# Kernel tuning notes

Hardware: AMD Instinct MI355X
Metric: run time of the kernel (lower is better)

Reference implementation:

```python
import jax, jax.numpy as jnp
import numpy as np
import math

B, S, D, H = 4, 2048, 512, 8
DK = D // H
EPS = 1e-6

def _xavier(key, shape):
    fan_in, fan_out = shape[1], shape[0]
    a = math.sqrt(6.0 / (fan_in + fan_out))
    return jax.random.uniform(key, shape, jnp.float32, -a, a)

def setup_inputs() -> dict:
    key = jax.random.key(0)
    ks = jax.random.split(key, 8)
    return {
        "x_q": jax.random.normal(ks[0], (B, S, D), jnp.float32),
        "x_k": jax.random.normal(ks[1], (B, S, D), jnp.float32),
        "Wq": _xavier(ks[2], (D, D)),
        "Wk": _xavier(ks[3], (D, D)),
        "Wv": _xavier(ks[4], (D, D)),
        "Wg": jnp.zeros((D, D), jnp.float32),      # gating weight init to 0
        "bg": jnp.ones((D,), jnp.float32),          # gating bias init to 1
        "Wo": _xavier(ks[5], (D, D)),
        "bo": jnp.zeros((D,), jnp.float32),
        "gamma": jnp.ones((D,), jnp.float32),
        "beta": jnp.zeros((D,), jnp.float32),
    }

def _ln(x, gamma, beta):
    mu = jnp.mean(x, axis=-1, keepdims=True)
    var = jnp.var(x, axis=-1, keepdims=True)
    return (x - mu) * jax.lax.rsqrt(var + EPS) * gamma + beta

def reference(x_q, x_k, Wq, Wk, Wv, Wg, bg, Wo, bo, gamma, beta):
    xq = _ln(x_q, gamma, beta)          # [B,S,D]
    xk = _ln(x_k, gamma, beta)
    q = xq @ Wq.T                        # nn.Linear: x @ W^T (no bias)
    k = xk @ Wk.T
    v = xk @ Wv.T
    q = q.reshape(B, S, H, DK)
    k = k.reshape(B, S, H, DK)
    v = v.reshape(B, S, H, DK)
    attn = jnp.einsum('bshd,bthd->bhst', q, k) / math.sqrt(DK)  # [B,H,S,S]
    attn = jax.nn.softmax(attn, axis=-1) * jax.nn.softmax(attn, axis=-2)
    out = jnp.einsum('bhst,bthd->bshd', attn, v).reshape(B, S, D)
    gate = jax.nn.sigmoid(xq @ Wg.T + bg)
    return (out * gate) @ Wo.T + bo
```

## Files before the change

kernel.cpp:

```cpp
#include <hip/hip_runtime.h>

#define BB 4
#define SS 2048
#define DD 512
#define HH 8
#define RR (BB * SS)
#define BH (BB * HH)

typedef unsigned short u16;
typedef unsigned int   u32;
typedef __attribute__((ext_vector_type(4))) float f32x4;
typedef __attribute__((ext_vector_type(8))) short bf16x8;

__device__ __forceinline__ float bf2f(u16 u) { return __uint_as_float(((u32)u) << 16); }
__device__ __forceinline__ u16 f2bf(float f) {
    u32 x = __float_as_uint(f);
    return (u16)((x + 0x7fffu + ((x >> 16) & 1u)) >> 16);
}
__device__ __forceinline__ bool is_bf16(const void* gamma) {
    return *(const u32*)gamma == 0x3F803F80u;
}
__device__ __forceinline__ float ldin(const void* p, size_t i, bool b16) {
    return b16 ? bf2f(((const u16*)p)[i]) : ((const float*)p)[i];
}
__device__ __forceinline__ float expc(float x) { return __expf(fminf(x, 60.f)); }

__global__ __launch_bounds__(256) void k_ln(
    const void* xq, const void* xk, const void* gamma, const void* beta,
    u16* __restrict__ lnq, u16* __restrict__ lnk, float* l_col)
{
    bool b16 = is_bf16(gamma);
    int row = blockIdx.x, tid = threadIdx.x;
    const void* x = blockIdx.y ? xk : xq;
    u16* o = blockIdx.y ? lnk : lnq;
    size_t base = (size_t)row * DD;

    if (blockIdx.y == 0 && row < 256) l_col[row * 256 + tid] = 0.f;

    float x0 = ldin(x, base + tid * 2, b16);
    float x1 = ldin(x, base + tid * 2 + 1, b16);
    float s = x0 + x1, ss = x0 * x0 + x1 * x1;
    for (int m = 1; m < 64; m <<= 1) { s += __shfl_xor(s, m); ss += __shfl_xor(ss, m); }
    __shared__ float ws4[4], wss4[4], mu_s, rs_s;
    int wv = tid >> 6;
    if ((tid & 63) == 0) { ws4[wv] = s; wss4[wv] = ss; }
    __syncthreads();
    if (tid == 0) {
        float S1 = ws4[0] + ws4[1] + ws4[2] + ws4[3];
        float S2 = wss4[0] + wss4[1] + wss4[2] + wss4[3];
        float mu = S1 / (float)DD;
        float var = S2 / (float)DD - mu * mu;
        mu_s = mu; rs_s = rsqrtf(fmaxf(var, 0.f) + 1e-6f);
    }
    __syncthreads();
    float mu = mu_s, rstd = rs_s;
    float g0 = ldin(gamma, tid * 2, b16), g1 = ldin(gamma, tid * 2 + 1, b16);
    float b0 = ldin(beta, tid * 2, b16),  b1 = ldin(beta, tid * 2 + 1, b16);
    o[base + tid * 2]     = f2bf((x0 - mu) * rstd * g0 + b0);
    o[base + tid * 2 + 1] = f2bf((x1 - mu) * rstd * g1 + b1);
}

__global__ __launch_bounds__(256) void k_proj4(
    const u16* __restrict__ lnq, const u16* __restrict__ lnk,
    const void* Wq, const void* Wk, const void* Wv, const void* Wg,
    const void* bg, const void* gamma,
    u16* __restrict__ qb, u16* __restrict__ kb,
    u16* __restrict__ vT, u16* __restrict__ gb)
{
    __shared__ __align__(16) u16 As[128][64];
    __shared__ __align__(16) u16 Bs[128][64];
    bool b16 = is_bf16(gamma);
    int which = blockIdx.z;
    const u16* A = (which <= 1) ? lnq : lnk;
    const void* W = (which == 0) ? Wq : (which == 1) ? Wg : (which == 2) ? Wk : Wv;
    u16* C = (which == 0) ? qb : (which == 1) ? gb : (which == 2) ? kb : vT;

    int tid = threadIdx.x;
    int lane = tid & 63, wave = tid >> 6;
    int r = lane & 15, q4 = lane >> 4;
    int m0 = blockIdx.y * 128, n0 = blockIdx.x * 128;
    int moff = (wave >> 1) * 64, noff = (wave & 1) * 64;
    const int K = DD, N = DD;

    f32x4 acc[4][4];
    for (int i = 0; i < 4; ++i)
        for (int j = 0; j < 4; ++j) acc[i][j] = (f32x4){0.f, 0.f, 0.f, 0.f};

    for (int k0 = 0; k0 < K; k0 += 64) {
        #pragma unroll
        for (int t = 0; t < 4; ++t) {
            int e = t * 2048 + tid * 8;
            int row = e >> 6, kk = e & 63;
            int ksw = kk ^ ((row & 7) * 8);
            *(uint4*)&As[row][ksw] = *(const uint4*)&A[(size_t)(m0 + row) * K + k0 + kk];
            if (b16) {
                *(uint4*)&Bs[row][ksw] =
                    *(const uint4*)&((const u16*)W)[(size_t)(n0 + row) * K + k0 + kk];
            } else {
                const float* wp = (const float*)W + (size_t)(n0 + row) * K + k0 + kk;
                float4 w0 = *(const float4*)wp;
                float4 w1 = *(const float4*)(wp + 4);
                ushort4 lo, hi;
                lo.x = f2bf(w0.x); lo.y = f2bf(w0.y); lo.z = f2bf(w0.z); lo.w = f2bf(w0.w);
                hi.x = f2bf(w1.x); hi.y = f2bf(w1.y); hi.z = f2bf(w1.z); hi.w = f2bf(w1.w);
                *(ushort4*)&Bs[row][ksw] = lo;
                *(ushort4*)&Bs[row][ksw + 4] = hi;
            }
        }
        __syncthreads();
        #pragma unroll
        for (int ksp = 0; ksp < 2; ++ksp) {
            int kb2 = ksp * 32 + q4 * 8;
            bf16x8 af[4], bfr[4];
            #pragma unroll
            for (int i = 0; i < 4; ++i) {
                int rowm = moff + i * 16 + r;
                af[i] = *(const bf16x8*)&As[rowm][kb2 ^ ((rowm & 7) * 8)];
                int rown = noff + i * 16 + r;
                bfr[i] = *(const bf16x8*)&Bs[rown][kb2 ^ ((rown & 7) * 8)];
            }
            #pragma unroll
            for (int i = 0; i < 4; ++i)
                #pragma unroll
                for (int j = 0; j < 4; ++j)
                    acc[i][j] = __builtin_amdgcn_mfma_f32_16x16x32_bf16(af[i], bfr[j], acc[i][j], 0, 0, 0);
        }
        __syncthreads();
    }

    if (which == 3) {
        int b = m0 >> 11;
        int sb = (m0 & 2047) + moff + q4 * 4;
        #pragma unroll
        for (int j = 0; j < 4; ++j) {
            int n = n0 + noff + j * 16 + r;
            int h = n >> 6, dkl = n & 63;
            size_t vbase = (((size_t)b * 8 + h) * 64 + dkl) * SS;
            #pragma unroll
            for (int i = 0; i < 4; ++i) {
                ushort4 wv;
                wv.x = f2bf(acc[i][j][0]); wv.y = f2bf(acc[i][j][1]);
                wv.z = f2bf(acc[i][j][2]); wv.w = f2bf(acc[i][j][3]);
                *(ushort4*)&C[vbase + sb + i * 16] = wv;
            }
        }
    } else {
        #pragma unroll
        for (int j = 0; j < 4; ++j) {
            int col = n0 + noff + j * 16 + r;
            float bj = (which == 1) ? ldin(bg, col, b16) : 0.f;
            #pragma unroll
            for (int i = 0; i < 4; ++i) {
                int rowb = m0 + moff + i * 16 + q4 * 4;
                #pragma unroll
                for (int g = 0; g < 4; ++g) {
                    float v = acc[i][j][g];
                    if (which == 1) v = 1.f / (1.f + expc(-(v + bj)));
                    C[(size_t)(rowb + g) * N + col] = f2bf(v);
                }
            }
        }
    }
}

__global__ __launch_bounds__(256) void k_sum(
    const u16* __restrict__ qm, const u16* __restrict__ km,
    float* __restrict__ l_row, float* __restrict__ l_col)
{
    __shared__ __align__(16) u16 Qs[64][64];
    __shared__ __align__(16) u16 Ks[128][64];
    __shared__ float colS[128];
    int tid = threadIdx.x, lane = tid & 63, wave = tid >> 6;
    int r = lane & 15, q4 = lane >> 4;
    int s0 = blockIdx.x * 64;
    int bh = blockIdx.y, b = bh >> 3, h = bh & 7;
    size_t hb = (size_t)b * SS * DD + (size_t)h * 64;

    #pragma unroll
    for (int t = 0; t < 2; ++t) {
        int e = t * 2048 + tid * 8;
        int row = e >> 6, kk = e & 63;
        *(uint4*)&Qs[row][kk ^ ((row & 7) * 8)] = *(const uint4*)&qm[hb + (size_t)(s0 + row) * DD + kk];
    }
    if (tid < 128) colS[tid] = 0.f;
    __syncthreads();

    int moff = wave * 16;
    bf16x8 aq[2];
    #pragma unroll
    for (int ksp = 0; ksp < 2; ++ksp) {
        int rowm = moff + r;
        aq[ksp] = *(const bf16x8*)&Qs[rowm][(ksp * 32 + q4 * 8) ^ ((rowm & 7) * 8)];
    }

    float rs[4] = {};
    for (int t0 = 0; t0 < SS; t0 += 128) {
        #pragma unroll
        for (int t = 0; t < 4; ++t) {
            int e = t * 2048 + tid * 8;
            int row = e >> 6, kk = e & 63;
            *(uint4*)&Ks[row][kk ^ ((row & 7) * 8)] = *(const uint4*)&km[hb + (size_t)(t0 + row) * DD + kk];
        }
        __syncthreads();

        f32x4 acc[8];
        for (int j = 0; j < 8; ++j) acc[j] = (f32x4){0.f, 0.f, 0.f, 0.f};
        #pragma unroll
        for (int ksp = 0; ksp < 2; ++ksp) {
            int kb2 = ksp * 32 + q4 * 8;
            bf16x8 bk[8];
            #pragma unroll
            for (int j = 0; j < 8; ++j) {
                int n = j * 16 + r;
                bk[j] = *(const bf16x8*)&Ks[n][kb2 ^ ((n & 7) * 8)];
            }
            #pragma unroll
            for (int j = 0; j < 8; ++j)
                acc[j] = __builtin_amdgcn_mfma_f32_16x16x32_bf16(aq[ksp], bk[j], acc[j], 0, 0, 0);
        }

        float cv[8];
        #pragma unroll
        for (int j = 0; j < 8; ++j) {
            cv[j] = 0.f;
            #pragma unroll
            for (int g = 0; g < 4; ++g) {
                float ev = expc(acc[j][g] * 0.125f);
                rs[g] += ev;
                cv[j] += ev;
            }
        }
        #pragma unroll
        for (int j = 0; j < 8; ++j) {
            float v = cv[j];
            v += __shfl_xor(v, 16); v += __shfl_xor(v, 32);
            if (q4 == 0) atomicAdd(&colS[j * 16 + r], v);
        }
        __syncthreads();
        if (tid < 128) {
            atomicAdd(&l_col[(size_t)bh * SS + t0 + tid], colS[tid]);
            colS[tid] = 0.f;
        }
        __syncthreads();
    }
    #pragma unroll
    for (int g = 0; g < 4; ++g) {
        float v = rs[g];
        v += __shfl_xor(v, 1); v += __shfl_xor(v, 2);
        v += __shfl_xor(v, 4); v += __shfl_xor(v, 8);
        if (r == 0) l_row[(size_t)bh * SS + s0 + moff + q4 * 4 + g] = v;
    }
}

__global__ void k_rcp(const float* __restrict__ l_row, const float* __restrict__ l_col,
                      float* __restrict__ inv_r, float* __restrict__ inv_c, int n)
{
    int i = blockIdx.x * blockDim.x + threadIdx.x;
    if (i < n) {
        inv_r[i] = 1.f / fmaxf(l_row[i], 1e-30f);
        inv_c[i] = 1.f / fmaxf(l_col[i], 1e-30f);
    }
}

__global__ __launch_bounds__(256) void k_pv(
    const u16* __restrict__ qm, const u16* __restrict__ km, const u16* __restrict__ vT,
    const float* __restrict__ inv_r, const float* __restrict__ inv_c,
    const u16* __restrict__ gate, u16* __restrict__ og)
{
    __shared__ __align__(16) u16 Ep[64][128];
    __shared__ __align__(16) u16 KV[8192];
    int tid = threadIdx.x, lane = tid & 63, wave = tid >> 6;
    int r = lane & 15, q4 = lane >> 4;
    int s0 = blockIdx.x * 64;
    int bh = blockIdx.y, b = bh >> 3, h = bh & 7;
    size_t hb = (size_t)b * SS * DD + (size_t)h * 64;
    int moff = wave * 16;

    #pragma unroll
    for (int t = 0; t < 2; ++t) {
        int e = t * 2048 + tid * 8;
        int row = e >> 6, kk = e & 63;
        *(uint4*)&Ep[row][kk ^ ((row & 7) * 8)] = *(const uint4*)&qm[hb + (size_t)(s0 + row) * DD + kk];
    }
    __syncthreads();
    bf16x8 aq[2];
    #pragma unroll
    for (int ksp = 0; ksp < 2; ++ksp) {
        int rowm = moff + r;
        aq[ksp] = *(const bf16x8*)&Ep[rowm][(ksp * 32 + q4 * 8) ^ ((rowm & 7) * 8)];
    }
    __syncthreads();

    f32x4 acco[4];
    for (int j = 0; j < 4; ++j) acco[j] = (f32x4){0.f, 0.f, 0.f, 0.f};

    for (int t0 = 0; t0 < SS; t0 += 128) {
        #pragma unroll
        for (int t = 0; t < 4; ++t) {
            int e = t * 2048 + tid * 8;
            int row = e >> 6, kk = e & 63;
            *(uint4*)&KV[row * 64 + (kk ^ ((row & 7) * 8))] =
                *(const uint4*)&km[hb + (size_t)(t0 + row) * DD + kk];
        }
        __syncthreads();

        f32x4 accs[8];
        for (int j = 0; j < 8; ++j) accs[j] = (f32x4){0.f, 0.f, 0.f, 0.f};
        #pragma unroll
        for (int ksp = 0; ksp < 2; ++ksp) {
            int kb2 = ksp * 32 + q4 * 8;
            bf16x8 bk[8];
            #pragma unroll
            for (int j = 0; j < 8; ++j) {
                int n = j * 16 + r;
                bk[j] = *(const bf16x8*)&KV[n * 64 + (kb2 ^ ((n & 7) * 8))];
            }
            #pragma unroll
            for (int j = 0; j < 8; ++j)
                accs[j] = __builtin_amdgcn_mfma_f32_16x16x32_bf16(aq[ksp], bk[j], accs[j], 0, 0, 0);
        }
        __syncthreads();

        #pragma unroll
        for (int c = 0; c < 4; ++c) {
            int e = c * 256 + tid;
            int row = e >> 4, tc = (e & 15) * 8;
            *(uint4*)&KV[row * 128 + (tc ^ ((row & 7) * 8))] =
                *(const uint4*)&vT[((size_t)bh * 64 + row) * SS + t0 + tc];
        }
        #pragma unroll
        for (int j = 0; j < 8; ++j) {
            float icj = inv_c[(size_t)bh * SS + t0 + j * 16 + r];
            int srow = moff + q4 * 4;
            #pragma unroll
            for (int g = 0; g < 4; ++g) {
                float pv = expc(accs[j][g] * 0.25f) * icj;
                int sl = srow + g, tl = j * 16 + r;
                Ep[sl][tl ^ ((sl & 7) * 8)] = f2bf(pv);
            }
        }
        __syncthreads();

        #pragma unroll
        for (int ksp = 0; ksp < 4; ++ksp) {
            int kb2 = ksp * 32 + q4 * 8;
            int sl = moff + r;
            bf16x8 ap = *(const bf16x8*)&Ep[sl][kb2 ^ ((sl & 7) * 8)];
            bf16x8 bv[4];
            #pragma unroll
            for (int j = 0; j < 4; ++j) {
                int n = j * 16 + r;
                bv[j] = *(const bf16x8*)&KV[n * 128 + (kb2 ^ ((n & 7) * 8))];
            }
            #pragma unroll
            for (int j = 0; j < 4; ++j)
                acco[j] = __builtin_amdgcn_mfma_f32_16x16x32_bf16(ap, bv[j], acco[j], 0, 0, 0);
        }
        __syncthreads();
    }

    #pragma unroll
    for (int g = 0; g < 4; ++g) {
        int srow = s0 + moff + q4 * 4 + g;
        float ir = inv_r[(size_t)bh * SS + srow];
        size_t ob = (size_t)b * SS * DD + (size_t)srow * DD + (size_t)h * 64;
        #pragma unroll
        for (int j = 0; j < 4; ++j) {
            int dk = j * 16 + r;
            og[ob + dk] = f2bf(acco[j][g] * ir * bf2f(gate[ob + dk]));
        }
    }
}

__global__ __launch_bounds__(256) void k_gemm_out(
    const u16* __restrict__ A, const void* W, const void* gamma,
    float* __restrict__ Cf, const void* bias)
{
    __shared__ __align__(16) u16 As[128][64];
    __shared__ __align__(16) u16 Bs[128][64];
    bool b16 = is_bf16(gamma);
    int tid = threadIdx.x;
    int lane = tid & 63, wave = tid >> 6;
    int r = lane & 15, q4 = lane >> 4;
    int m0 = blockIdx.y * 128, n0 = blockIdx.x * 128;
    int moff = (wave >> 1) * 64, noff = (wave & 1) * 64;
    const int K = DD, N = DD;

    f32x4 acc[4][4];
    for (int i = 0; i < 4; ++i)
        for (int j = 0; j < 4; ++j) acc[i][j] = (f32x4){0.f, 0.f, 0.f, 0.f};

    for (int k0 = 0; k0 < K; k0 += 64) {
        #pragma unroll
        for (int t = 0; t < 4; ++t) {
            int e = t * 2048 + tid * 8;
            int row = e >> 6, kk = e & 63;
            int ksw = kk ^ ((row & 7) * 8);
            *(uint4*)&As[row][ksw] = *(const uint4*)&A[(size_t)(m0 + row) * K + k0 + kk];
            if (b16) {
                *(uint4*)&Bs[row][ksw] =
                    *(const uint4*)&((const u16*)W)[(size_t)(n0 + row) * K + k0 + kk];
            } else {
                const float* wp = (const float*)W + (size_t)(n0 + row) * K + k0 + kk;
                float4 w0 = *(const float4*)wp;
                float4 w1 = *(const float4*)(wp + 4);
                ushort4 lo, hi;
                lo.x = f2bf(w0.x); lo.y = f2bf(w0.y); lo.z = f2bf(w0.z); lo.w = f2bf(w0.w);
                hi.x = f2bf(w1.x); hi.y = f2bf(w1.y); hi.z = f2bf(w1.z); hi.w = f2bf(w1.w);
                *(ushort4*)&Bs[row][ksw] = lo;
                *(ushort4*)&Bs[row][ksw + 4] = hi;
            }
        }
        __syncthreads();
        #pragma unroll
        for (int ksp = 0; ksp < 2; ++ksp) {
            int kb2 = ksp * 32 + q4 * 8;
            bf16x8 af[4], bfr[4];
            #pragma unroll
            for (int i = 0; i < 4; ++i) {
                int rowm = moff + i * 16 + r;
                af[i] = *(const bf16x8*)&As[rowm][kb2 ^ ((rowm & 7) * 8)];
                int rown = noff + i * 16 + r;
                bfr[i] = *(const bf16x8*)&Bs[rown][kb2 ^ ((rown & 7) * 8)];
            }
            #pragma unroll
            for (int i = 0; i < 4; ++i)
                #pragma unroll
                for (int j = 0; j < 4; ++j)
                    acc[i][j] = __builtin_amdgcn_mfma_f32_16x16x32_bf16(af[i], bfr[j], acc[i][j], 0, 0, 0);
        }
        __syncthreads();
    }
    #pragma unroll
    for (int j = 0; j < 4; ++j) {
        int col = n0 + noff + j * 16 + r;
        float bj = ldin(bias, col, b16);
        #pragma unroll
        for (int i = 0; i < 4; ++i) {
            int rowb = m0 + moff + i * 16 + q4 * 4;
            #pragma unroll
            for (int g = 0; g < 4; ++g) {
                float v = acc[i][j][g] + bj;
                size_t idx = (size_t)(rowb + g) * N + col;
                if (b16) ((u16*)Cf)[idx] = f2bf(v);
                else     Cf[idx] = v;
            }
        }
    }
}

extern "C" void kernel_launch(void* const* d_in, const int* in_sizes, int n_in,
                              void* d_out, int out_size, void* d_ws, size_t ws_size,
                              hipStream_t stream)
{
    const void* x_q   = d_in[0];
    const void* x_k   = d_in[1];
    const void* Wq    = d_in[2];
    const void* Wk    = d_in[3];
    const void* Wv    = d_in[4];
    const void* Wg    = d_in[5];
    const void* bg    = d_in[6];
    const void* Wo    = d_in[7];
    const void* bo    = d_in[8];
    const void* gamma = d_in[9];
    const void* beta  = d_in[10];

    char* base = (char*)d_ws;
    u16* lnq = (u16*)(base);
    u16* lnk = (u16*)(base + (size_t) 8 * 1024 * 1024);
    u16* qb  = (u16*)(base + (size_t)16 * 1024 * 1024);
    u16* kb  = (u16*)(base + (size_t)24 * 1024 * 1024);
    u16* gb  = (u16*)(base + (size_t)32 * 1024 * 1024);
    float* l_row = (float*)(base + (size_t)40 * 1024 * 1024);
    float* l_col = (float*)(base + (size_t)40 * 1024 * 1024 + 262144);
    float* inv_r = (float*)(base + (size_t)40 * 1024 * 1024 + 524288);
    float* inv_c = (float*)(base + (size_t)40 * 1024 * 1024 + 786432);
    u16* vT = (u16*)d_out;
    u16* og = lnk;

    k_ln<<<dim3(RR, 2), 256, 0, stream>>>(x_q, x_k, gamma, beta, lnq, lnk, l_col);

    k_proj4<<<dim3(4, 64, 4), 256, 0, stream>>>(lnq, lnk, Wq, Wk, Wv, Wg, bg, gamma,
                                                qb, kb, vT, gb);

    k_sum<<<dim3(SS / 64, BH), 256, 0, stream>>>(qb, kb, l_row, l_col);
    k_rcp<<<dim3(BH * SS / 256), 256, 0, stream>>>(l_row, l_col, inv_r, inv_c, BH * SS);
    k_pv<<<dim3(SS / 64, BH), 256, 0, stream>>>(qb, kb, vT, inv_r, inv_c, gb, og);

    k_gemm_out<<<dim3(4, 64), 256, 0, stream>>>(og, Wo, gamma, (float*)d_out, bo);
}
```

Before: 359.2 us.

## Compute row and column softmax sums in separate passes, drop atomics and rcp kernel

The sum kernel now runs a second grid slice that swaps Q and K, so column sums come from row-reduction of K·Qᵀ instead of shared and global atomics. The reciprocal is folded into the sum kernel, which removes the k_rcp launch and the l_col zeroing in the LayerNorm kernel. k_pv gets separate padded K and V tiles so both loads are issued before a single barrier, and shared-memory rows are padded. The cost is that the QK score matmul and exp are done twice in the sum stage instead of once, in exchange for removing the atomic contention and some barriers.

```diff
diff --git a/kernel.cpp b/kernel.cpp
--- a/kernel.cpp
+++ b/kernel.cpp
@@ -27,15 +27,13 @@
 
 __global__ __launch_bounds__(256) void k_ln(
     const void* xq, const void* xk, const void* gamma, const void* beta,
-    u16* __restrict__ lnq, u16* __restrict__ lnk, float* l_col)
+    u16* __restrict__ lnq, u16* __restrict__ lnk)
 {
     bool b16 = is_bf16(gamma);
     int row = blockIdx.x, tid = threadIdx.x;
     const void* x = blockIdx.y ? xk : xq;
     u16* o = blockIdx.y ? lnk : lnq;
     size_t base = (size_t)row * DD;
-
-    if (blockIdx.y == 0 && row < 256) l_col[row * 256 + tid] = 0.f;
 
     float x0 = ldin(x, base + tid * 2, b16);
     float x1 = ldin(x, base + tid * 2 + 1, b16);
@@ -163,26 +161,28 @@
     }
 }
 
-__global__ __launch_bounds__(256) void k_sum(
-    const u16* __restrict__ qm, const u16* __restrict__ km,
-    float* __restrict__ l_row, float* __restrict__ l_col)
-{
-    __shared__ __align__(16) u16 Qs[64][64];
-    __shared__ __align__(16) u16 Ks[128][64];
-    __shared__ float colS[128];
+__global__ __launch_bounds__(256) void k_sum2(
+    const u16* __restrict__ qb, const u16* __restrict__ kb,
+    float* __restrict__ invR, float* __restrict__ invC)
+{
+    __shared__ __align__(16) u16 As[64 * 72];
+    __shared__ __align__(16) u16 Bs[128 * 72];
     int tid = threadIdx.x, lane = tid & 63, wave = tid >> 6;
     int r = lane & 15, q4 = lane >> 4;
     int s0 = blockIdx.x * 64;
     int bh = blockIdx.y, b = bh >> 3, h = bh & 7;
+    const u16* A = blockIdx.z ? kb : qb;
+    const u16* B = blockIdx.z ? qb : kb;
+    float* out = blockIdx.z ? invC : invR;
     size_t hb = (size_t)b * SS * DD + (size_t)h * 64;
 
     #pragma unroll
     for (int t = 0; t < 2; ++t) {
         int e = t * 2048 + tid * 8;
         int row = e >> 6, kk = e & 63;
-        *(uint4*)&Qs[row][kk ^ ((row & 7) * 8)] = *(const uint4*)&qm[hb + (size_t)(s0 + row) * DD + kk];
-    }
-    if (tid < 128) colS[tid] = 0.f;
+        *(uint4*)&As[row * 72 + (kk ^ ((row & 7) * 8))] =
+            *(const uint4*)&A[hb + (size_t)(s0 + row) * DD + kk];
+    }
     __syncthreads();
 
     int moff = wave * 16;
@@ -190,8 +190,9 @@
     #pragma unroll
     for (int ksp = 0; ksp < 2; ++ksp) {
         int rowm = moff + r;
-        aq[ksp] = *(const bf16x8*)&Qs[rowm][(ksp * 32 + q4 * 8) ^ ((rowm & 7) * 8)];
-    }
+        aq[ksp] = *(const bf16x8*)&As[rowm * 72 + ((ksp * 32 + q4 * 8) ^ ((rowm & 7) * 8))];
+    }
+    __syncthreads();
 
     float rs[4] = {};
     for (int t0 = 0; t0 < SS; t0 += 128) {
@@ -199,47 +200,33 @@
         for (int t = 0; t < 4; ++t) {
             int e = t * 2048 + tid * 8;
             int row = e >> 6, kk = e & 63;
-            *(uint4*)&Ks[row][kk ^ ((row & 7) * 8)] = *(const uint4*)&km[hb + (size_t)(t0 + row) * DD + kk];
-        }
-        __syncthreads();
-
-        f32x4 acc[8];
-        for (int j = 0; j < 8; ++j) acc[j] = (f32x4){0.f, 0.f, 0.f, 0.f};
-        #pragma unroll
-        for (int ksp = 0; ksp < 2; ++ksp) {
-            int kb2 = ksp * 32 + q4 * 8;
-            bf16x8 bk[8];
-            #pragma unroll
-            for (int j = 0; j < 8; ++j) {
-                int n = j * 16 + r;
-                bk[j] = *(const bf16x8*)&Ks[n][kb2 ^ ((n & 7) * 8)];
-            }
-            #pragma unroll
-            for (int j = 0; j < 8; ++j)
-                acc[j] = __builtin_amdgcn_mfma_f32_16x16x32_bf16(aq[ksp], bk[j], acc[j], 0, 0, 0);
-        }
-
-        float cv[8];
-        #pragma unroll
-        for (int j = 0; j < 8; ++j) {
-            cv[j] = 0.f;
-            #pragma unroll
-            for (int g = 0; g < 4; ++g) {
-                float ev = expc(acc[j][g] * 0.125f);
-                rs[g] += ev;
-                cv[j] += ev;
-            }
-        }
-        #pragma unroll
-        for (int j = 0; j < 8; ++j) {
-            float v = cv[j];
-            v += __shfl_xor(v, 16); v += __shfl_xor(v, 32);
-            if (q4 == 0) atomicAdd(&colS[j * 16 + r], v);
-        }
-        __syncthreads();
-        if (tid < 128) {
-            atomicAdd(&l_col[(size_t)bh * SS + t0 + tid], colS[tid]);
-            colS[tid] = 0.f;
+            *(uint4*)&Bs[row * 72 + (kk ^ ((row & 7) * 8))] =
+                *(const uint4*)&B[hb + (size_t)(t0 + row) * DD + kk];
+        }
+        __syncthreads();
+
+        #pragma unroll
+        for (int jh = 0; jh < 2; ++jh) {
+            f32x4 accs[4];
+            for (int j = 0; j < 4; ++j) accs[j] = (f32x4){0.f, 0.f, 0.f, 0.f};
+            #pragma unroll
+            for (int ksp = 0; ksp < 2; ++ksp) {
+                int kb2 = ksp * 32 + q4 * 8;
+                bf16x8 bk[4];
+                #pragma unroll
+                for (int j = 0; j < 4; ++j) {
+                    int n = (jh * 4 + j) * 16 + r;
+                    bk[j] = *(const bf16x8*)&Bs[n * 72 + (kb2 ^ ((n & 7) * 8))];
+                }
+                #pragma unroll
+                for (int j = 0; j < 4; ++j)
+                    accs[j] = __builtin_amdgcn_mfma_f32_16x16x32_bf16(aq[ksp], bk[j], accs[j], 0, 0, 0);
+            }
+            #pragma unroll
+            for (int j = 0; j < 4; ++j)
+                #pragma unroll
+                for (int g = 0; g < 4; ++g)
+                    rs[g] += expc(accs[j][g] * 0.125f);
         }
         __syncthreads();
     }
@@ -248,27 +235,18 @@
         float v = rs[g];
         v += __shfl_xor(v, 1); v += __shfl_xor(v, 2);
         v += __shfl_xor(v, 4); v += __shfl_xor(v, 8);
-        if (r == 0) l_row[(size_t)bh * SS + s0 + moff + q4 * 4 + g] = v;
-    }
-}
-
-__global__ void k_rcp(const float* __restrict__ l_row, const float* __restrict__ l_col,
-                      float* __restrict__ inv_r, float* __restrict__ inv_c, int n)
-{
-    int i = blockIdx.x * blockDim.x + threadIdx.x;
-    if (i < n) {
-        inv_r[i] = 1.f / fmaxf(l_row[i], 1e-30f);
-        inv_c[i] = 1.f / fmaxf(l_col[i], 1e-30f);
+        if (r == 0) out[(size_t)bh * SS + s0 + moff + q4 * 4 + g] = 1.f / fmaxf(v, 1e-30f);
     }
 }
 
 __global__ __launch_bounds__(256) void k_pv(
     const u16* __restrict__ qm, const u16* __restrict__ km, const u16* __restrict__ vT,
-    const float* __restrict__ inv_r, const float* __restrict__ inv_c,
+    const float* __restrict__ invR, const float* __restrict__ invC,
     const u16* __restrict__ gate, u16* __restrict__ og)
 {
-    __shared__ __align__(16) u16 Ep[64][128];
-    __shared__ __align__(16) u16 KV[8192];
+    __shared__ __align__(16) u16 Ep[64 * 136];
+    __shared__ __align__(16) u16 Ks[128 * 72];
+    __shared__ __align__(16) u16 Vt[64 * 136];
     int tid = threadIdx.x, lane = tid & 63, wave = tid >> 6;
     int r = lane & 15, q4 = lane >> 4;
     int s0 = blockIdx.x * 64;
@@ -280,14 +258,15 @@
     for (int t = 0; t < 2; ++t) {
         int e = t * 2048 + tid * 8;
         int row = e >> 6, kk = e & 63;
-        *(uint4*)&Ep[row][kk ^ ((row & 7) * 8)] = *(const uint4*)&qm[hb + (size_t)(s0 + row) * DD + kk];
+        *(uint4*)&Ep[row * 136 + (kk ^ ((row & 7) * 8))] =
+            *(const uint4*)&qm[hb + (size_t)(s0 + row) * DD + kk];
     }
     __syncthreads();
     bf16x8 aq[2];
     #pragma unroll
     for (int ksp = 0; ksp < 2; ++ksp) {
         int rowm = moff + r;
-        aq[ksp] = *(const bf16x8*)&Ep[rowm][(ksp * 32 + q4 * 8) ^ ((rowm & 7) * 8)];
+        aq[ksp] = *(const bf16x8*)&Ep[rowm * 136 + ((ksp * 32 + q4 * 8) ^ ((rowm & 7) * 8))];
     }
     __syncthreads();
 
@@ -299,58 +278,59 @@
         for (int t = 0; t < 4; ++t) {
             int e = t * 2048 + tid * 8;
             int row = e >> 6, kk = e & 63;
-            *(uint4*)&KV[row * 64 + (kk ^ ((row & 7) * 8))] =
+            *(uint4*)&Ks[row * 72 + (kk ^ ((row & 7) * 8))] =
                 *(const uint4*)&km[hb + (size_t)(t0 + row) * DD + kk];
         }
-        __syncthreads();
-
-        f32x4 accs[8];
-        for (int j = 0; j < 8; ++j) accs[j] = (f32x4){0.f, 0.f, 0.f, 0.f};
-        #pragma unroll
-        for (int ksp = 0; ksp < 2; ++ksp) {
-            int kb2 = ksp * 32 + q4 * 8;
-            bf16x8 bk[8];
-            #pragma unroll
-            for (int j = 0; j < 8; ++j) {
-                int n = j * 16 + r;
-                bk[j] = *(const bf16x8*)&KV[n * 64 + (kb2 ^ ((n & 7) * 8))];
-            }
-            #pragma unroll
-            for (int j = 0; j < 8; ++j)
-                accs[j] = __builtin_amdgcn_mfma_f32_16x16x32_bf16(aq[ksp], bk[j], accs[j], 0, 0, 0);
-        }
-        __syncthreads();
-
         #pragma unroll
         for (int c = 0; c < 4; ++c) {
             int e = c * 256 + tid;
             int row = e >> 4, tc = (e & 15) * 8;
-            *(uint4*)&KV[row * 128 + (tc ^ ((row & 7) * 8))] =
+            *(uint4*)&Vt[row * 136 + (tc ^ ((row & 7) * 8))] =
                 *(const uint4*)&vT[((size_t)bh * 64 + row) * SS + t0 + tc];
         }
-        #pragma unroll
-        for (int j = 0; j < 8; ++j) {
-            float icj = inv_c[(size_t)bh * SS + t0 + j * 16 + r];
-            int srow = moff + q4 * 4;
-            #pragma unroll
-            for (int g = 0; g < 4; ++g) {
-                float pv = expc(accs[j][g] * 0.25f) * icj;
-                int sl = srow + g, tl = j * 16 + r;
-                Ep[sl][tl ^ ((sl & 7) * 8)] = f2bf(pv);
-            }
-        }
-        __syncthreads();
+        __syncthreads();
+
+        #pragma unroll
+        for (int jh = 0; jh < 2; ++jh) {
+            f32x4 accs[4];
+            for (int j = 0; j < 4; ++j) accs[j] = (f32x4){0.f, 0.f, 0.f, 0.f};
+            #pragma unroll
+            for (int ksp = 0; ksp < 2; ++ksp) {
+                int kb2 = ksp * 32 + q4 * 8;
+                bf16x8 bk[4];
+                #pragma unroll
+                for (int j = 0; j < 4; ++j) {
+                    int n = (jh * 4 + j) * 16 + r;
+                    bk[j] = *(const bf16x8*)&Ks[n * 72 + (kb2 ^ ((n & 7) * 8))];
+                }
+                #pragma unroll
+                for (int j = 0; j < 4; ++j)
+                    accs[j] = __builtin_amdgcn_mfma_f32_16x16x32_bf16(aq[ksp], bk[j], accs[j], 0, 0, 0);
+            }
+            #pragma unroll
+            for (int j = 0; j < 4; ++j) {
+                int jg = jh * 4 + j;
+                float icj = invC[(size_t)bh * SS + t0 + jg * 16 + r];
+                int srow = moff + q4 * 4;
+                #pragma unroll
+                for (int g = 0; g < 4; ++g) {
+                    float pv = expc(accs[j][g] * 0.25f) * icj;
+                    int sl = srow + g, tl = jg * 16 + r;
+                    Ep[sl * 136 + (tl ^ ((sl & 7) * 8))] = f2bf(pv);
+                }
+            }
+        }
 
         #pragma unroll
         for (int ksp = 0; ksp < 4; ++ksp) {
             int kb2 = ksp * 32 + q4 * 8;
             int sl = moff + r;
-            bf16x8 ap = *(const bf16x8*)&Ep[sl][kb2 ^ ((sl & 7) * 8)];
+            bf16x8 ap = *(const bf16x8*)&Ep[sl * 136 + (kb2 ^ ((sl & 7) * 8))];
             bf16x8 bv[4];
             #pragma unroll
             for (int j = 0; j < 4; ++j) {
                 int n = j * 16 + r;
-                bv[j] = *(const bf16x8*)&KV[n * 128 + (kb2 ^ ((n & 7) * 8))];
+                bv[j] = *(const bf16x8*)&Vt[n * 136 + (kb2 ^ ((n & 7) * 8))];
             }
             #pragma unroll
             for (int j = 0; j < 4; ++j)
@@ -362,7 +342,7 @@
     #pragma unroll
     for (int g = 0; g < 4; ++g) {
         int srow = s0 + moff + q4 * 4 + g;
-        float ir = inv_r[(size_t)bh * SS + srow];
+        float ir = invR[(size_t)bh * SS + srow];
         size_t ob = (size_t)b * SS * DD + (size_t)srow * DD + (size_t)h * 64;
         #pragma unroll
         for (int j = 0; j < 4; ++j) {
@@ -471,21 +451,19 @@
     u16* qb  = (u16*)(base + (size_t)16 * 1024 * 1024);
     u16* kb  = (u16*)(base + (size_t)24 * 1024 * 1024);
     u16* gb  = (u16*)(base + (size_t)32 * 1024 * 1024);
-    float* l_row = (float*)(base + (size_t)40 * 1024 * 1024);
-    float* l_col = (float*)(base + (size_t)40 * 1024 * 1024 + 262144);
-    float* inv_r = (float*)(base + (size_t)40 * 1024 * 1024 + 524288);
-    float* inv_c = (float*)(base + (size_t)40 * 1024 * 1024 + 786432);
+    float* invR = (float*)(base + (size_t)40 * 1024 * 1024);
+    float* invC = (float*)(base + (size_t)40 * 1024 * 1024 + 262144);
     u16* vT = (u16*)d_out;
     u16* og = lnk;
 
-    k_ln<<<dim3(RR, 2), 256, 0, stream>>>(x_q, x_k, gamma, beta, lnq, lnk, l_col);
+    k_ln<<<dim3(RR, 2), 256, 0, stream>>>(x_q, x_k, gamma, beta, lnq, lnk);
 
     k_proj4<<<dim3(4, 64, 4), 256, 0, stream>>>(lnq, lnk, Wq, Wk, Wv, Wg, bg, gamma,
                                                 qb, kb, vT, gb);
 
-    k_sum<<<dim3(SS / 64, BH), 256, 0, stream>>>(qb, kb, l_row, l_col);
-    k_rcp<<<dim3(BH * SS / 256), 256, 0, stream>>>(l_row, l_col, inv_r, inv_c, BH * SS);
-    k_pv<<<dim3(SS / 64, BH), 256, 0, stream>>>(qb, kb, vT, inv_r, inv_c, gb, og);
+    k_sum2<<<dim3(SS / 64, BH, 2), 256, 0, stream>>>(qb, kb, invR, invC);
+
+    k_pv<<<dim3(SS / 64, BH), 256, 0, stream>>>(qb, kb, vT, invR, invC, gb, og);
 
     k_gemm_out<<<dim3(4, 64), 256, 0, stream>>>(og, Wo, gamma, (float*)d_out, bo);
 }
```

Result: slower. 466.0 us (+29.8%).
